# Kernel tuning notes

Hardware: AMD Instinct MI355X
Metric: run time of the kernel (lower is better)

The kernel has to match this reference:

```python
import jax, jax.numpy as jnp
import numpy as np

N = 100000
SAMPLE = 25
FEAT = 128
HIDDEN = 128
CLASSES = 40


def setup_inputs() -> dict:
    key = jax.random.key(0)
    k_x, k_n, k_w1, k_w2, k_wl = jax.random.split(key, 5)
    X = jax.random.normal(k_x, (N, FEAT), dtype=jnp.float32)
    neighbors = jax.random.randint(k_n, (N, SAMPLE), 0, N, dtype=jnp.int32)
    # torch Linear weights are [out_features, in_features], xavier-uniform init
    def xavier(k, out_d, in_d):
        bound = float(np.sqrt(6.0 / (in_d + out_d)))
        return jax.random.uniform(k, (out_d, in_d), dtype=jnp.float32, minval=-bound, maxval=bound)
    W1 = xavier(k_w1, HIDDEN, FEAT)
    W2 = xavier(k_w2, HIDDEN, HIDDEN)
    Wlast = xavier(k_wl, CLASSES, HIDDEN)
    return {"X": X, "neighbors": neighbors, "W1": W1, "W2": W2, "Wlast": Wlast}


def reference(X, neighbors, W1, W2, Wlast):
    # forward: for each layer W: X = spmm(adj, X); X = X @ W.T; relu(X)
    # adj row i has sample_num entries of value 1/sample_num -> mean over sampled neighbors
    h = X
    for W in (W1, W2):
        agg = jnp.mean(h[neighbors], axis=1)          # [N, sample, d] -> [N, d]
        h = jax.nn.relu(jnp.einsum('nd,hd->nh', agg, W))
    return jnp.einsum('nh,ch->nc', h, Wlast)          # [N, class_num]
```

## Files before the change

### kernel.cpp

```cpp
#include <hip/hip_runtime.h>
#include <cstdint>
#include <cstddef>

typedef unsigned short u16;
typedef __bf16 bf16x8 __attribute__((ext_vector_type(8)));
typedef u16 u16x8 __attribute__((ext_vector_type(8)));
typedef float f32x4 __attribute__((ext_vector_type(4)));

#define N_NODES 100000
#define SAMPLE 25
#define FEAT 128
#define CLASSES 40

__device__ __forceinline__ float bf2f(u16 v) {
    return __uint_as_float(((unsigned)v) << 16);
}
__device__ __forceinline__ u16 f2bf(float f) {
    unsigned u = __float_as_uint(f);
    u += 0x7FFFu + ((u >> 16) & 1u);
    return (u16)(u >> 16);
}
__device__ __forceinline__ void split_bf(float x, u16& hi, u16& lo) {
    hi = f2bf(x);
    lo = f2bf(x - bf2f(hi));
}

__device__ __forceinline__ void split8(const float* ap, bf16x8& ah, bf16x8& al) {
    union { u16x8 u; bf16x8 b; } H, L;
    #pragma unroll
    for (int j = 0; j < 8; ++j) {
        u16 h, lo; split_bf(ap[j], h, lo);
        H.u[j] = h; L.u[j] = lo;
    }
    ah = H.b; al = L.b;
}

__device__ __forceinline__ f32x4 mfma_split(bf16x8 ah, bf16x8 al,
                                            bf16x8 bh, bf16x8 bl, f32x4 acc) {
    acc = __builtin_amdgcn_mfma_f32_16x16x32_bf16(ah, bh, acc, 0, 0, 0);
    acc = __builtin_amdgcn_mfma_f32_16x16x32_bf16(al, bh, acc, 0, 0, 0);
    acc = __builtin_amdgcn_mfma_f32_16x16x32_bf16(ah, bl, acc, 0, 0, 0);
    return acc;
}

__global__ __launch_bounds__(256) void prep_weights(
    const float* __restrict__ W1, const float* __restrict__ W2,
    const float* __restrict__ Wl,
    u16* __restrict__ w1h, u16* __restrict__ w1l,
    u16* __restrict__ w2h, u16* __restrict__ w2l,
    u16* __restrict__ wlh, u16* __restrict__ wll)
{
    const int i = blockIdx.x * 256 + threadIdx.x;
    const int stride = gridDim.x * 256;
    for (int j = i; j < FEAT * FEAT; j += stride) {
        split_bf(W1[j], w1h[j], w1l[j]);
        split_bf(W2[j], w2h[j], w2l[j]);
    }
    for (int j = i; j < CLASSES * FEAT; j += stride) {
        split_bf(Wl[j], wlh[j], wll[j]);
    }
}

#define NPB32 32
#define ZT_STRIDE 136
#define SBATCH 5

__global__ __launch_bounds__(128, 4) void k1_gemm(
    const float* __restrict__ X,
    const u16* __restrict__ w1h, const u16* __restrict__ w1l,
    u16* __restrict__ Z1)
{
    __shared__ u16 zt[NPB32][ZT_STRIDE];

    const int t = threadIdx.x;
    const int w  = t >> 6;
    const int l  = t & 63;
    const int lr = l & 15;
    const int lq = l >> 4;
    const int blockStart = blockIdx.x * NPB32;
    const float* Xrow = X + (size_t)(blockStart + w * 16 + lr) * FEAT;

    bf16x8 ah[4], al[4];
    #pragma unroll
    for (int k = 0; k < 4; ++k) {
        f32x4 x0 = *(const f32x4*)(Xrow + k * 32 + lq * 8);
        f32x4 x1 = *(const f32x4*)(Xrow + k * 32 + lq * 8 + 4);
        float tmp[8];
        #pragma unroll
        for (int j = 0; j < 4; ++j) { tmp[j] = x0[j]; tmp[4 + j] = x1[j]; }
        split8(tmp, ah[k], al[k]);
    }

    #pragma unroll
    for (int c = 0; c < 8; ++c) {
        f32x4 acc = {0.f, 0.f, 0.f, 0.f};
        #pragma unroll
        for (int k = 0; k < 4; ++k) {
            const size_t off = (size_t)(c * 16 + lr) * FEAT + k * 32 + lq * 8;
            bf16x8 bh = *(const bf16x8*)(w1h + off);
            bf16x8 bl = *(const bf16x8*)(w1l + off);
            acc = mfma_split(ah[k], al[k], bh, bl, acc);
        }
        #pragma unroll
        for (int r = 0; r < 4; ++r)
            zt[w * 16 + lq * 4 + r][c * 16 + lr] = f2bf(acc[r]);
    }
    __syncthreads();

    #pragma unroll
    for (int p = 0; p < 4; ++p) {
        const int idx = p * 128 + t;
        const int row = idx >> 4;
        const int col = (idx & 15) * 8;
        *(u16x8*)(Z1 + (size_t)(blockStart + row) * FEAT + col) =
            *(const u16x8*)&zt[row][col];
    }
}

__device__ __forceinline__ void gather_afrag(
    const u16* __restrict__ Zin, const int* __restrict__ myn, int lq,
    bf16x8 (&ah)[4], bf16x8 (&al)[4])
{
    float acc[4][8];
    #pragma unroll
    for (int k = 0; k < 4; ++k)
        #pragma unroll
        for (int j = 0; j < 8; ++j) acc[k][j] = 0.f;

    #pragma unroll 1
    for (int b = 0; b < SAMPLE / SBATCH; ++b) {
        u16x8 buf[SBATCH][4];
        #pragma unroll
        for (int s = 0; s < SBATCH; ++s) {
            const u16* row = Zin + ((size_t)myn[b * SBATCH + s] << 7) + lq * 8;
            buf[s][0] = *(const u16x8*)(row);
            buf[s][1] = *(const u16x8*)(row + 32);
            buf[s][2] = *(const u16x8*)(row + 64);
            buf[s][3] = *(const u16x8*)(row + 96);
        }
        #pragma unroll
        for (int s = 0; s < SBATCH; ++s)
            #pragma unroll
            for (int k = 0; k < 4; ++k)
                #pragma unroll
                for (int j = 0; j < 8; ++j) acc[k][j] += bf2f(buf[s][k][j]);
    }

    #pragma unroll
    for (int k = 0; k < 4; ++k) {
        float tmp[8];
        #pragma unroll
        for (int j = 0; j < 8; ++j) {
            float m = acc[k][j] * (1.0f / SAMPLE);
            tmp[j] = m > 0.f ? m : 0.f;
        }
        split8(tmp, ah[k], al[k]);
    }
}

__global__ __launch_bounds__(128, 2) void k2_hop(
    const u16* __restrict__ Zin, const int* __restrict__ nb,
    const u16* __restrict__ wh, const u16* __restrict__ wl,
    u16* __restrict__ Zout)
{
    __shared__ int nbs[NPB32 * SAMPLE];
    __shared__ u16 zt[NPB32][ZT_STRIDE];

    const int t = threadIdx.x;
    const int blockStart = blockIdx.x * NPB32;

    for (int i = t; i < NPB32 * SAMPLE; i += 128)
        nbs[i] = nb[blockStart * SAMPLE + i];
    __syncthreads();

    const int w  = t >> 6;
    const int l  = t & 63;
    const int lr = l & 15;
    const int lq = l >> 4;

    bf16x8 ah[4], al[4];
    gather_afrag(Zin, &nbs[(w * 16 + lr) * SAMPLE], lq, ah, al);

    #pragma unroll
    for (int c = 0; c < 8; ++c) {
        f32x4 o = {0.f, 0.f, 0.f, 0.f};
        #pragma unroll
        for (int k = 0; k < 4; ++k) {
            const size_t off = (size_t)(c * 16 + lr) * FEAT + k * 32 + lq * 8;
            bf16x8 bh = *(const bf16x8*)(wh + off);
            bf16x8 bl = *(const bf16x8*)(wl + off);
            o = mfma_split(ah[k], al[k], bh, bl, o);
        }
        #pragma unroll
        for (int r = 0; r < 4; ++r)
            zt[w * 16 + lq * 4 + r][c * 16 + lr] = f2bf(o[r]);
    }
    __syncthreads();

    #pragma unroll
    for (int p = 0; p < 4; ++p) {
        const int idx = p * 128 + t;
        const int row = idx >> 4;
        const int col = (idx & 15) * 8;
        *(u16x8*)(Zout + (size_t)(blockStart + row) * FEAT + col) =
            *(const u16x8*)&zt[row][col];
    }
}

__global__ __launch_bounds__(128, 2) void k3_hop(
    const u16* __restrict__ Zin, const int* __restrict__ nb,
    const u16* __restrict__ wh, const u16* __restrict__ wl,
    float* __restrict__ out)
{
    __shared__ int nbs[NPB32 * SAMPLE];

    const int t = threadIdx.x;
    const int blockStart = blockIdx.x * NPB32;

    for (int i = t; i < NPB32 * SAMPLE; i += 128)
        nbs[i] = nb[blockStart * SAMPLE + i];
    __syncthreads();

    const int w  = t >> 6;
    const int l  = t & 63;
    const int lr = l & 15;
    const int lq = l >> 4;

    bf16x8 ah[4], al[4];
    gather_afrag(Zin, &nbs[(w * 16 + lr) * SAMPLE], lq, ah, al);

    #pragma unroll
    for (int c = 0; c < 3; ++c) {
        const int o = c * 16 + lr;
        f32x4 a = {0.f, 0.f, 0.f, 0.f};
        #pragma unroll
        for (int k = 0; k < 4; ++k) {
            bf16x8 bh, bl;
            if (o < CLASSES) {
                const size_t off = (size_t)o * FEAT + k * 32 + lq * 8;
                bh = *(const bf16x8*)(wh + off);
                bl = *(const bf16x8*)(wl + off);
            } else {
                #pragma unroll
                for (int j = 0; j < 8; ++j) { bh[j] = (__bf16)0.f; bl[j] = (__bf16)0.f; }
            }
            a = mfma_split(ah[k], al[k], bh, bl, a);
        }
        if (o < CLASSES) {
            #pragma unroll
            for (int r = 0; r < 4; ++r) {
                const int node = blockStart + w * 16 + lq * 4 + r;
                out[(size_t)node * CLASSES + o] = a[r];
            }
        }
    }
}

#define NPB 64
#define AGG_STRIDE 136

__global__ __launch_bounds__(256) void gnn_layer1(
    const float* __restrict__ X, const int* __restrict__ nb,
    const u16* __restrict__ w1h, const u16* __restrict__ w1l,
    u16* __restrict__ h1)
{
    __shared__ int nbs[NPB * SAMPLE];
    __shared__ u16 agg_h[NPB][AGG_STRIDE];
    __shared__ u16 agg_l[NPB][AGG_STRIDE];

    const int t = threadIdx.x;
    const int blockStart = blockIdx.x * NPB;

    for (int i = t; i < NPB * SAMPLE; i += 256) {
        int gi = blockStart * SAMPLE + i;
        if (gi >= N_NODES * SAMPLE) gi = N_NODES * SAMPLE - 1;
        nbs[i] = nb[gi];
    }
    __syncthreads();

    for (int item = t; item < NPB * 16; item += 256) {
        const int nl = item >> 4;
        const int fg = item & 15;
        float acc[8];
        #pragma unroll
        for (int j = 0; j < 8; ++j) acc[j] = 0.f;
        const int* myn = &nbs[nl * SAMPLE];
        for (int s = 0; s < SAMPLE; ++s) {
            const float4* p = (const float4*)(X + (size_t)myn[s] * FEAT + fg * 8);
            float4 a = p[0], b = p[1];
            acc[0] += a.x; acc[1] += a.y; acc[2] += a.z; acc[3] += a.w;
            acc[4] += b.x; acc[5] += b.y; acc[6] += b.z; acc[7] += b.w;
        }
        u16x8 oh, ol;
        #pragma unroll
        for (int j = 0; j < 8; ++j) {
            float m = acc[j] * (1.0f / SAMPLE);
            u16 h, lo; split_bf(m, h, lo);
            oh[j] = h; ol[j] = lo;
        }
        *(u16x8*)&agg_h[nl][fg * 8] = oh;
        *(u16x8*)&agg_l[nl][fg * 8] = ol;
    }
    __syncthreads();

    const int w  = t >> 6;
    const int l  = t & 63;
    const int lr = l & 15;
    const int lq = l >> 4;

    bf16x8 ah[4], al[4];
    #pragma unroll
    for (int k = 0; k < 4; ++k) {
        ah[k] = *(const bf16x8*)&agg_h[w * 16 + lr][k * 32 + lq * 8];
        al[k] = *(const bf16x8*)&agg_l[w * 16 + lr][k * 32 + lq * 8];
    }

    #pragma unroll
    for (int c = 0; c < 8; ++c) {
        f32x4 acc = {0.f, 0.f, 0.f, 0.f};
        #pragma unroll
        for (int k = 0; k < 4; ++k) {
            const size_t off = (size_t)(c * 16 + lr) * FEAT + k * 32 + lq * 8;
            bf16x8 bh = *(const bf16x8*)(w1h + off);
            bf16x8 bl = *(const bf16x8*)(w1l + off);
            acc = mfma_split(ah[k], al[k], bh, bl, acc);
        }
        #pragma unroll
        for (int r = 0; r < 4; ++r) {
            int node = blockStart + w * 16 + lq * 4 + r;
            if (node < N_NODES) {
                float v = acc[r] > 0.f ? acc[r] : 0.f;
                h1[(size_t)node * FEAT + c * 16 + lr] = f2bf(v);
            }
        }
    }
}

__global__ __launch_bounds__(256) void gnn_layer2_final(
    const u16* __restrict__ h1, const int* __restrict__ nb,
    const u16* __restrict__ w2h, const u16* __restrict__ w2l,
    const u16* __restrict__ wlh, const u16* __restrict__ wll,
    float* __restrict__ out)
{
    __shared__ int nbs[NPB * SAMPLE];
    __shared__ u16 agg_h[NPB][AGG_STRIDE];
    __shared__ u16 agg_l[NPB][AGG_STRIDE];

    const int t = threadIdx.x;
    const int blockStart = blockIdx.x * NPB;

    for (int i = t; i < NPB * SAMPLE; i += 256) {
        int gi = blockStart * SAMPLE + i;
        if (gi >= N_NODES * SAMPLE) gi = N_NODES * SAMPLE - 1;
        nbs[i] = nb[gi];
    }
    __syncthreads();

    for (int item = t; item < NPB * 16; item += 256) {
        const int nl = item >> 4;
        const int fg = item & 15;
        float acc[8];
        #pragma unroll
        for (int j = 0; j < 8; ++j) acc[j] = 0.f;
        const int* myn = &nbs[nl * SAMPLE];
        for (int s = 0; s < SAMPLE; ++s) {
            u16x8 v = *(const u16x8*)(h1 + (size_t)myn[s] * FEAT + fg * 8);
            #pragma unroll
            for (int j = 0; j < 8; ++j) acc[j] += bf2f(v[j]);
        }
        u16x8 oh, ol;
        #pragma unroll
        for (int j = 0; j < 8; ++j) {
            float m = acc[j] * (1.0f / SAMPLE);
            u16 h, lo; split_bf(m, h, lo);
            oh[j] = h; ol[j] = lo;
        }
        *(u16x8*)&agg_h[nl][fg * 8] = oh;
        *(u16x8*)&agg_l[nl][fg * 8] = ol;
    }
    __syncthreads();

    const int w  = t >> 6;
    const int l  = t & 63;
    const int lr = l & 15;
    const int lq = l >> 4;

    f32x4 hacc[8];
    {
        bf16x8 ah[4], al[4];
        #pragma unroll
        for (int k = 0; k < 4; ++k) {
            ah[k] = *(const bf16x8*)&agg_h[w * 16 + lr][k * 32 + lq * 8];
            al[k] = *(const bf16x8*)&agg_l[w * 16 + lr][k * 32 + lq * 8];
        }
        #pragma unroll
        for (int c = 0; c < 8; ++c) {
            f32x4 acc = {0.f, 0.f, 0.f, 0.f};
            #pragma unroll
            for (int k = 0; k < 4; ++k) {
                const size_t off = (size_t)(c * 16 + lr) * FEAT + k * 32 + lq * 8;
                bf16x8 bh = *(const bf16x8*)(w2h + off);
                bf16x8 bl = *(const bf16x8*)(w2l + off);
                acc = mfma_split(ah[k], al[k], bh, bl, acc);
            }
            hacc[c] = acc;
        }
    }
    __syncthreads();

    #pragma unroll
    for (int c = 0; c < 8; ++c) {
        #pragma unroll
        for (int r = 0; r < 4; ++r) {
            float v = hacc[c][r] > 0.f ? hacc[c][r] : 0.f;
            u16 h, l2; split_bf(v, h, l2);
            agg_h[w * 16 + lq * 4 + r][c * 16 + lr] = h;
            agg_l[w * 16 + lq * 4 + r][c * 16 + lr] = l2;
        }
    }
    __syncthreads();

    {
        bf16x8 ah[4], al[4];
        #pragma unroll
        for (int k = 0; k < 4; ++k) {
            ah[k] = *(const bf16x8*)&agg_h[w * 16 + lr][k * 32 + lq * 8];
            al[k] = *(const bf16x8*)&agg_l[w * 16 + lr][k * 32 + lq * 8];
        }
        #pragma unroll
        for (int c = 0; c < 3; ++c) {
            const int o = c * 16 + lr;
            f32x4 acc = {0.f, 0.f, 0.f, 0.f};
            #pragma unroll
            for (int k = 0; k < 4; ++k) {
                bf16x8 bh, bl;
                if (o < CLASSES) {
                    const size_t off = (size_t)o * FEAT + k * 32 + lq * 8;
                    bh = *(const bf16x8*)(wlh + off);
                    bl = *(const bf16x8*)(wll + off);
                } else {
                    #pragma unroll
                    for (int j = 0; j < 8; ++j) { bh[j] = (__bf16)0.f; bl[j] = (__bf16)0.f; }
                }
                acc = mfma_split(ah[k], al[k], bh, bl, acc);
            }
            if (o < CLASSES) {
                #pragma unroll
                for (int r = 0; r < 4; ++r) {
                    int node = blockStart + w * 16 + lq * 4 + r;
                    if (node < N_NODES) {
                        out[(size_t)node * CLASSES + o] = acc[r];
                    }
                }
            }
        }
    }
}

extern "C" void kernel_launch(void* const* d_in, const int* in_sizes, int n_in,
                              void* d_out, int out_size, void* d_ws, size_t ws_size,
                              hipStream_t stream) {
    const float* X  = (const float*)d_in[0];
    const int*   nb = (const int*)d_in[1];
    const float* W1 = (const float*)d_in[2];
    const float* W2 = (const float*)d_in[3];
    const float* Wl = (const float*)d_in[4];
    float* out = (float*)d_out;

    const size_t zelems = (size_t)N_NODES * FEAT;
    const size_t welems = 4 * (size_t)FEAT * FEAT + 2 * (size_t)CLASSES * FEAT;
    const size_t need_fast = (2 * zelems + welems) * sizeof(u16);

    if (ws_size >= need_fast) {
        u16* Z1  = (u16*)d_ws;
        u16* Z2  = Z1 + zelems;
        u16* w1h = Z2 + zelems;
        u16* w1l = w1h + FEAT * FEAT;
        u16* w2h = w1l + FEAT * FEAT;
        u16* w2l = w2h + FEAT * FEAT;
        u16* wlh = w2l + FEAT * FEAT;
        u16* wll = wlh + CLASSES * FEAT;

        prep_weights<<<64, 256, 0, stream>>>(W1, W2, Wl, w1h, w1l, w2h, w2l, wlh, wll);
        const int blocks = N_NODES / NPB32;
        k1_gemm<<<blocks, 128, 0, stream>>>(X, w1h, w1l, Z1);
        k2_hop<<<blocks, 128, 0, stream>>>(Z1, nb, w2h, w2l, Z2);
        k3_hop<<<blocks, 128, 0, stream>>>(Z2, nb, wlh, wll, out);
    } else {
        u16* h1  = (u16*)d_ws;
        u16* w1h = h1 + zelems;
        u16* w1l = w1h + FEAT * FEAT;
        u16* w2h = w1l + FEAT * FEAT;
        u16* w2l = w2h + FEAT * FEAT;
        u16* wlh = w2l + FEAT * FEAT;
        u16* wll = wlh + CLASSES * FEAT;

        prep_weights<<<64, 256, 0, stream>>>(W1, W2, Wl, w1h, w1l, w2h, w2l, wlh, wll);
        const int blocks = (N_NODES + NPB - 1) / NPB;
        gnn_layer1<<<blocks, 256, 0, stream>>>(X, nb, w1h, w1l, h1);
        gnn_layer2_final<<<blocks, 256, 0, stream>>>(h1, nb, w2h, w2l, wlh, wll, out);
    }
}
```

Before: 373.6 us.

## Gather neighbor rows via global_load_lds DMA into LDS with single-wave blocks

Replaces the register-based neighbor gather in the two hop kernels with direct global-to-LDS DMA loads (global_load_lds), staging all 25 sampled rows for 4 nodes at a time and then reducing them from LDS. Blocks shrink to one 64-thread wave handling 16 nodes, and the aggregated hi/lo bf16 fragments pass through LDS before the MFMA stage. The aim is to cut VGPR pressure and issue overhead in the gather and to keep more loads in flight. The cost is a larger LDS footprint per block (about 25KB staging plus agg buffers), which limits occupancy, plus a full waitcnt after each batch that serialises load and reduce.

```diff
diff --git a/kernel.cpp b/kernel.cpp
--- a/kernel.cpp
+++ b/kernel.cpp
@@ -43,6 +43,13 @@
     return acc;
 }
 
+__device__ __forceinline__ void dma16(const void* gsrc, void* ldst) {
+    __builtin_amdgcn_global_load_lds(
+        (__attribute__((address_space(1))) void*)gsrc,
+        (__attribute__((address_space(3))) void*)ldst,
+        16, 0, 0);
+}
+
 __global__ __launch_bounds__(256) void prep_weights(
     const float* __restrict__ W1, const float* __restrict__ W2,
     const float* __restrict__ Wl,
@@ -63,7 +70,8 @@
 
 #define NPB32 32
 #define ZT_STRIDE 136
-#define SBATCH 5
+#define NPW 16
+#define AGG_ST 136
 
 __global__ __launch_bounds__(128, 4) void k1_gemm(
     const float* __restrict__ X,
@@ -117,69 +125,83 @@
     }
 }
 
-__device__ __forceinline__ void gather_afrag(
-    const u16* __restrict__ Zin, const int* __restrict__ myn, int lq,
-    bf16x8 (&ah)[4], bf16x8 (&al)[4])
-{
-    float acc[4][8];
-    #pragma unroll
-    for (int k = 0; k < 4; ++k)
-        #pragma unroll
-        for (int j = 0; j < 8; ++j) acc[k][j] = 0.f;
+__device__ __forceinline__ void gather_dma(
+    const u16* __restrict__ Zin, const int* __restrict__ nbs,
+    u16* __restrict__ stage,
+    u16* __restrict__ aggH,
+    u16* __restrict__ aggL,
+    int l)
+{
+    const int gn = l & 3;
+    const int gf = l >> 2;
 
     #pragma unroll 1
-    for (int b = 0; b < SAMPLE / SBATCH; ++b) {
-        u16x8 buf[SBATCH][4];
-        #pragma unroll
-        for (int s = 0; s < SBATCH; ++s) {
-            const u16* row = Zin + ((size_t)myn[b * SBATCH + s] << 7) + lq * 8;
-            buf[s][0] = *(const u16x8*)(row);
-            buf[s][1] = *(const u16x8*)(row + 32);
-            buf[s][2] = *(const u16x8*)(row + 64);
-            buf[s][3] = *(const u16x8*)(row + 96);
-        }
-        #pragma unroll
-        for (int s = 0; s < SBATCH; ++s)
+    for (int c = 0; c < 4; ++c) {
+        const int* base = &nbs[(c * 4 + gn) * SAMPLE];
+        __builtin_amdgcn_sched_barrier(0);
+        #pragma unroll
+        for (int s = 0; s < SAMPLE; ++s) {
+            const u16* src = Zin + ((size_t)base[s] << 7) + (gf << 3);
+            dma16(src, &stage[s * 512]);
+        }
+        __builtin_amdgcn_sched_barrier(0);
+        __builtin_amdgcn_s_waitcnt(0);
+        __builtin_amdgcn_sched_barrier(0);
+
+        float acc[8];
+        #pragma unroll
+        for (int j = 0; j < 8; ++j) acc[j] = 0.f;
+        #pragma unroll
+        for (int s = 0; s < SAMPLE; ++s) {
+            u16x8 v = *(const u16x8*)&stage[s * 512 + l * 8];
             #pragma unroll
-            for (int k = 0; k < 4; ++k)
-                #pragma unroll
-                for (int j = 0; j < 8; ++j) acc[k][j] += bf2f(buf[s][k][j]);
-    }
-
-    #pragma unroll
-    for (int k = 0; k < 4; ++k) {
-        float tmp[8];
+            for (int j = 0; j < 8; ++j) acc[j] += bf2f(v[j]);
+        }
+
+        u16x8 oh, ol;
         #pragma unroll
         for (int j = 0; j < 8; ++j) {
-            float m = acc[k][j] * (1.0f / SAMPLE);
-            tmp[j] = m > 0.f ? m : 0.f;
-        }
-        split8(tmp, ah[k], al[k]);
-    }
-}
-
-__global__ __launch_bounds__(128, 2) void k2_hop(
+            float m = acc[j] * (1.0f / SAMPLE);
+            m = m > 0.f ? m : 0.f;
+            u16 h, lo; split_bf(m, h, lo);
+            oh[j] = h; ol[j] = lo;
+        }
+        const int nl = c * 4 + gn;
+        *(u16x8*)&aggH[nl * AGG_ST + gf * 8] = oh;
+        *(u16x8*)&aggL[nl * AGG_ST + gf * 8] = ol;
+    }
+}
+
+__global__ __launch_bounds__(64) void k2_hop(
     const u16* __restrict__ Zin, const int* __restrict__ nb,
     const u16* __restrict__ wh, const u16* __restrict__ wl,
     u16* __restrict__ Zout)
 {
-    __shared__ int nbs[NPB32 * SAMPLE];
-    __shared__ u16 zt[NPB32][ZT_STRIDE];
-
-    const int t = threadIdx.x;
-    const int blockStart = blockIdx.x * NPB32;
-
-    for (int i = t; i < NPB32 * SAMPLE; i += 128)
+    __shared__ int nbs[NPW * SAMPLE];
+    __shared__ __align__(16) u16 stage[SAMPLE * 512];
+    __shared__ __align__(16) u16 aggH[NPW * AGG_ST];
+    __shared__ __align__(16) u16 aggL[NPW * AGG_ST];
+    __shared__ __align__(16) u16 zt[NPW][FEAT];
+
+    const int l = threadIdx.x;
+    const int blockStart = blockIdx.x * NPW;
+
+    #pragma unroll
+    for (int i = l; i < NPW * SAMPLE; i += 64)
         nbs[i] = nb[blockStart * SAMPLE + i];
     __syncthreads();
 
-    const int w  = t >> 6;
-    const int l  = t & 63;
+    gather_dma(Zin, nbs, stage, aggH, aggL, l);
+
     const int lr = l & 15;
     const int lq = l >> 4;
 
     bf16x8 ah[4], al[4];
-    gather_afrag(Zin, &nbs[(w * 16 + lr) * SAMPLE], lq, ah, al);
+    #pragma unroll
+    for (int k = 0; k < 4; ++k) {
+        ah[k] = *(const bf16x8*)&aggH[lr * AGG_ST + k * 32 + lq * 8];
+        al[k] = *(const bf16x8*)&aggL[lr * AGG_ST + k * 32 + lq * 8];
+    }
 
     #pragma unroll
     for (int c = 0; c < 8; ++c) {
@@ -193,13 +215,13 @@
         }
         #pragma unroll
         for (int r = 0; r < 4; ++r)
-            zt[w * 16 + lq * 4 + r][c * 16 + lr] = f2bf(o[r]);
+            zt[lq * 4 + r][c * 16 + lr] = f2bf(o[r]);
     }
     __syncthreads();
 
     #pragma unroll
     for (int p = 0; p < 4; ++p) {
-        const int idx = p * 128 + t;
+        const int idx = p * 64 + l;
         const int row = idx >> 4;
         const int col = (idx & 15) * 8;
         *(u16x8*)(Zout + (size_t)(blockStart + row) * FEAT + col) =
@@ -207,27 +229,35 @@
     }
 }
 
-__global__ __launch_bounds__(128, 2) void k3_hop(
+__global__ __launch_bounds__(64) void k3_hop(
     const u16* __restrict__ Zin, const int* __restrict__ nb,
     const u16* __restrict__ wh, const u16* __restrict__ wl,
     float* __restrict__ out)
 {
-    __shared__ int nbs[NPB32 * SAMPLE];
-
-    const int t = threadIdx.x;
-    const int blockStart = blockIdx.x * NPB32;
-
-    for (int i = t; i < NPB32 * SAMPLE; i += 128)
+    __shared__ int nbs[NPW * SAMPLE];
+    __shared__ __align__(16) u16 stage[SAMPLE * 512];
+    __shared__ __align__(16) u16 aggH[NPW * AGG_ST];
+    __shared__ __align__(16) u16 aggL[NPW * AGG_ST];
+
+    const int l = threadIdx.x;
+    const int blockStart = blockIdx.x * NPW;
+
+    #pragma unroll
+    for (int i = l; i < NPW * SAMPLE; i += 64)
         nbs[i] = nb[blockStart * SAMPLE + i];
     __syncthreads();
 
-    const int w  = t >> 6;
-    const int l  = t & 63;
+    gather_dma(Zin, nbs, stage, aggH, aggL, l);
+
     const int lr = l & 15;
     const int lq = l >> 4;
 
     bf16x8 ah[4], al[4];
-    gather_afrag(Zin, &nbs[(w * 16 + lr) * SAMPLE], lq, ah, al);
+    #pragma unroll
+    for (int k = 0; k < 4; ++k) {
+        ah[k] = *(const bf16x8*)&aggH[lr * AGG_ST + k * 32 + lq * 8];
+        al[k] = *(const bf16x8*)&aggL[lr * AGG_ST + k * 32 + lq * 8];
+    }
 
     #pragma unroll
     for (int c = 0; c < 3; ++c) {
@@ -249,7 +279,7 @@
         if (o < CLASSES) {
             #pragma unroll
             for (int r = 0; r < 4; ++r) {
-                const int node = blockStart + w * 16 + lq * 4 + r;
+                const int node = blockStart + lq * 4 + r;
                 out[(size_t)node * CLASSES + o] = a[r];
             }
         }
@@ -482,10 +512,9 @@
         u16* wll = wlh + CLASSES * FEAT;
 
         prep_weights<<<64, 256, 0, stream>>>(W1, W2, Wl, w1h, w1l, w2h, w2l, wlh, wll);
-        const int blocks = N_NODES / NPB32;
-        k1_gemm<<<blocks, 128, 0, stream>>>(X, w1h, w1l, Z1);
-        k2_hop<<<blocks, 128, 0, stream>>>(Z1, nb, w2h, w2l, Z2);
-        k3_hop<<<blocks, 128, 0, stream>>>(Z2, nb, wlh, wll, out);
+        k1_gemm<<<N_NODES / NPB32, 128, 0, stream>>>(X, w1h, w1l, Z1);
+        k2_hop<<<N_NODES / NPW, 64, 0, stream>>>(Z1, nb, w2h, w2l, Z2);
+        k3_hop<<<N_NODES / NPW, 64, 0, stream>>>(Z2, nb, wlh, wll, out);
     } else {
         u16* h1  = (u16*)d_ws;
         u16* w1h = h1 + zelems;
```

Measured after the change: 395.4 us. 5.8% more time.
